# Performance work log

Hardware: AMD Instinct MI355X
Metric: run time of the kernel (lower is better)

The kernel has to match this reference:

```python
import jax, jax.numpy as jnp
import numpy as np

B, DM, DC, H = 16384, 1024, 8, 256  # batch, MRI feat dim, clinical feat dim, hidden_dim


def setup_inputs() -> dict:
    key = jax.random.key(0)
    ks = jax.random.split(key, 16)
    f = lambda k, s: jax.random.normal(k, s, dtype=jnp.float32)
    return {
        # encoder outputs (4 MRI modalities @1024-d, clinical @8-d)
        'feat_t1': f(ks[0], (B, DM)), 'feat_t1c': f(ks[1], (B, DM)),
        'feat_t2': f(ks[2], (B, DM)), 'feat_flair': f(ks[3], (B, DM)),
        'feat_cl': f(ks[4], (B, DC)),
        # per-modality projection Linears (MRI ones stacked: same math as 4 separate Linears)
        'Wp_mri': f(ks[5], (4, H, DM)) * 0.02, 'bp_mri': jnp.zeros((4, H), jnp.float32),
        'Wp_cl': f(ks[6], (H, DC)) * 0.02, 'bp_cl': jnp.zeros((H,), jnp.float32),
        # attention MLP: Linear(256,64) -> Tanh -> Linear(64,1)
        'Wa1': f(ks[7], (64, H)) * 0.02, 'ba1': jnp.zeros((64,), jnp.float32),
        'Wa2': f(ks[8], (1, 64)) * 0.02, 'ba2': jnp.zeros((1,), jnp.float32),
        # classifier: 256->128 LN ReLU -> 128->64 LN ReLU -> 64->1 (num_class-1)
        'Wc1': f(ks[9], (128, H)) * 0.02, 'bc1': jnp.zeros((128,), jnp.float32),
        'g1': jnp.ones((128,), jnp.float32), 'be1': jnp.zeros((128,), jnp.float32),
        'Wc2': f(ks[10], (64, 128)) * 0.02, 'bc2': jnp.zeros((64,), jnp.float32),
        'g2': jnp.ones((64,), jnp.float32), 'be2': jnp.zeros((64,), jnp.float32),
        'Wc3': f(ks[11], (1, 64)) * 0.02, 'bc3': jnp.zeros((1,), jnp.float32),
    }


def _ln(x, g, b, eps=1e-5):
    m = jnp.mean(x, axis=-1, keepdims=True)
    v = jnp.var(x, axis=-1, keepdims=True)
    return (x - m) * jax.lax.rsqrt(v + eps) * g + b


def reference(feat_t1, feat_t1c, feat_t2, feat_flair, feat_cl,
              Wp_mri, bp_mri, Wp_cl, bp_cl,
              Wa1, ba1, Wa2, ba2,
              Wc1, bc1, g1, be1, Wc2, bc2, g2, be2, Wc3, bc3):
    mri = jnp.stack([feat_t1, feat_t1c, feat_t2, feat_flair], axis=1)  # [B,4,DM]
    pm = jnp.einsum('bmd,mhd->bmh', mri, Wp_mri) + bp_mri              # [B,4,H] per-modality Linear
    pc = feat_cl @ Wp_cl.T + bp_cl                                     # [B,H]
    proj = jnp.concatenate([pm, pc[:, None, :]], axis=1)               # [B,5,H] == torch.stack(proj_feats, dim=1)
    scores = jnp.tanh(proj @ Wa1.T + ba1) @ Wa2.T + ba2                # [B,5,1]
    attn_weights = jax.nn.softmax(scores, axis=1)                      # softmax over modalities
    fused = jnp.sum(attn_weights * proj, axis=1)                       # [B,H]
    h = jax.nn.relu(_ln(fused @ Wc1.T + bc1, g1, be1))                 # dropout is identity in eval
    h = jax.nn.relu(_ln(h @ Wc2.T + bc2, g2, be2))
    out = h @ Wc3.T + bc3                                              # [B,1]
    return out, attn_weights
```

## Files before the change

### kernel.cpp

```cpp
#include <hip/hip_runtime.h>
#include <math.h>

typedef unsigned short u16;
typedef unsigned int   u32;
typedef __bf16 bf16x8 __attribute__((ext_vector_type(8)));
typedef float  f32x4  __attribute__((ext_vector_type(4)));
typedef u16    u16x8  __attribute__((ext_vector_type(8)));
typedef u16    u16x4  __attribute__((ext_vector_type(4)));

#define B_TOT 16384
#define DM_   1024
#define H_    256

#define WS_SCORES 41943040
#define WS_WP     42270720
#define WS_WA1    44367872
#define WS_WC1    44400640
#define WS_WC2    44466176

__device__ __forceinline__ u16 f2bf(float f){
  __bf16 h = (__bf16)f;
  return __builtin_bit_cast(u16, h);
}
__device__ __forceinline__ float bf2f(u16 h){
  return __builtin_bit_cast(float, ((u32)h) << 16);
}
__device__ __forceinline__ u16x4 cvt4(f32x4 a){
  u16x4 h;
  #pragma unroll
  for (int j = 0; j < 4; j++) h[j] = f2bf(a[j]);
  return h;
}
__device__ __forceinline__ f32x4 mfma16(bf16x8 a, bf16x8 b, f32x4 c){
  return __builtin_amdgcn_mfma_f32_16x16x32_bf16(a, b, c, 0, 0, 0);
}
__device__ __forceinline__ void glds16(const void* g, void* l){
  __builtin_amdgcn_global_load_lds(
      (const __attribute__((address_space(1))) void*)g,
      (__attribute__((address_space(3))) void*)l, 16, 0, 0);
}

__global__ void k0_convert(const float* __restrict__ s0, u16* __restrict__ d0, int n0,
                           const float* __restrict__ s1, u16* __restrict__ d1, int n1,
                           const float* __restrict__ s2, u16* __restrict__ d2, int n2,
                           const float* __restrict__ s3, u16* __restrict__ d3, int n3)
{
  int total4 = (n0 + n1 + n2 + n3) >> 2;
  for (int i = blockIdx.x * blockDim.x + threadIdx.x; i < total4; i += gridDim.x * blockDim.x){
    int e = i << 2;
    const float* s; u16* d; int off;
    if (e < n0)            { s = s0; d = d0; off = e; }
    else if (e < n0+n1)    { s = s1; d = d1; off = e - n0; }
    else if (e < n0+n1+n2) { s = s2; d = d2; off = e - n0 - n1; }
    else                   { s = s3; d = d3; off = e - n0 - n1 - n2; }
    f32x4 f = *(const f32x4*)(s + off);
    *(u16x4*)(d + off) = cvt4(f);
  }
}

__global__ __launch_bounds__(256) void k1b_clin(
    const float* __restrict__ fcl, const float* __restrict__ Wpcl, const float* __restrict__ bpcl,
    const u16* __restrict__ Wa1bf, const float* __restrict__ ba1,
    const float* __restrict__ Wa2, const float* __restrict__ ba2,
    u16* __restrict__ proj, float* __restrict__ scores)
{
  __shared__ u16 pcs[4][16*264];
  const int tid = threadIdx.x, lane = tid & 63, wv = tid >> 6;
  const int l15 = lane & 15, l4 = lane >> 4;
  const int rbase = blockIdx.x * 64 + wv * 16;

  f32x4 wA[4], wB[4];
  f32x4 bp = *(const f32x4*)(bpcl + lane * 4);
  #pragma unroll
  for (int c = 0; c < 4; c++){
    wA[c] = *(const f32x4*)(Wpcl + (lane*4 + c) * 8);
    wB[c] = *(const f32x4*)(Wpcl + (lane*4 + c) * 8 + 4);
  }
  #pragma unroll 4
  for (int r = 0; r < 16; r++){
    int row = rbase + r;
    f32x4 fA = *(const f32x4*)(fcl + (size_t)row * 8);
    f32x4 fB = *(const f32x4*)(fcl + (size_t)row * 8 + 4);
    u16x4 h;
    #pragma unroll
    for (int c = 0; c < 4; c++){
      float v = bp[c] + fA[0]*wA[c][0] + fA[1]*wA[c][1] + fA[2]*wA[c][2] + fA[3]*wA[c][3]
                      + fB[0]*wB[c][0] + fB[1]*wB[c][1] + fB[2]*wB[c][2] + fB[3]*wB[c][3];
      h[c] = f2bf(v);
    }
    *(u16x4*)(proj + (size_t)row * 1280 + 1024 + lane * 4) = h;
    *(u16x4*)(&pcs[wv][r * 264 + lane * 4]) = h;
  }
  f32x4 at[4];
  #pragma unroll
  for (int nf = 0; nf < 4; nf++) at[nf] = f32x4{0.f,0.f,0.f,0.f};
  #pragma unroll
  for (int kk = 0; kk < 8; kk++){
    bf16x8 a = *(const bf16x8*)((const char*)&pcs[wv][0] + l15*528 + kk*64 + l4*16);
    #pragma unroll
    for (int nf = 0; nf < 4; nf++){
      bf16x8 b = *(const bf16x8*)((const char*)Wa1bf + (nf*16 + l15)*512 + kk*64 + l4*16);
      at[nf] = mfma16(a, b, at[nf]);
    }
  }
  float po[4] = {0.f,0.f,0.f,0.f};
  #pragma unroll
  for (int nf = 0; nf < 4; nf++){
    int col = nf*16 + l15;
    float bb = ba1[col], w2 = Wa2[col];
    #pragma unroll
    for (int rg = 0; rg < 4; rg++) po[rg] += tanhf(at[nf][rg] + bb) * w2;
  }
  #pragma unroll
  for (int rg = 0; rg < 4; rg++){
    #pragma unroll
    for (int d = 1; d < 16; d <<= 1) po[rg] += __shfl_xor(po[rg], d);
  }
  if (l15 == 0){
    float b2 = ba2[0];
    #pragma unroll
    for (int rg = 0; rg < 4; rg++)
      scores[(size_t)(rbase + l4*4 + rg) * 5 + 4] = po[rg] + b2;
  }
}

__global__ __launch_bounds__(512, 4) void k1_proj(
    const float* __restrict__ ft1, const float* __restrict__ ft1c,
    const float* __restrict__ ft2, const float* __restrict__ ftfl,
    const u16* __restrict__ Wpbf, const float* __restrict__ bpm,
    const u16* __restrict__ Wa1bf, const float* __restrict__ ba1,
    const float* __restrict__ Wa2, const float* __restrict__ ba2,
    u16* __restrict__ proj, float* __restrict__ scores)
{
  extern __shared__ char lds[];
  const int bid = blockIdx.x;
  const int mm = (bid & 7) >> 1;
  const int bx = ((bid >> 3) << 1) | (bid & 1);
  const int b0 = bx * 64;
  const int tid = threadIdx.x;
  const int lane = tid & 63;
  const int wv = tid >> 6;
  const int l15 = lane & 15, l4 = lane >> 4;

  const float* Am = (mm == 0) ? ft1 : ((mm == 1) ? ft1c : ((mm == 2) ? ft2 : ftfl));
  const u16*   Wm = Wpbf + (size_t)mm * (H_ * DM_);
  const char*  Ab8 = (const char*)Am;

  const int a_r0 = tid >> 4;
  const int a_r1 = 32 + a_r0;
  const size_t a_src0 = (size_t)(b0 + a_r0) * 4096 + (size_t)((((tid & 15) * 16)) ^ ((a_r0 & 7) << 4));
  const size_t a_src1 = (size_t)(b0 + a_r1) * 4096 + (size_t)((((tid & 15) * 16)) ^ ((a_r1 & 7) << 4));
  const int a_dstw = wv * 1024;

  const u16* pW = Wm + (size_t)(wv*32 + l15) * DM_ + l4*8;

  u16x8 rW[2][4];
  f32x4 acc[4][2];
  #pragma unroll
  for (int i = 0; i < 4; i++)
    #pragma unroll
    for (int j = 0; j < 2; j++) acc[i][j] = f32x4{0.f,0.f,0.f,0.f};

  #pragma unroll
  for (int q = 0; q < 4; q++){
    int nf = q >> 1, kk = q & 1;
    rW[0][q] = *(const u16x8*)(pW + (size_t)nf*16*DM_ + kk*32);
  }
  #pragma unroll
  for (int t = 0; t < 3; t++){
    char* base = lds + t * 16384;
    glds16(Ab8 + a_src0 + (size_t)t * 256, base + a_dstw);
    glds16(Ab8 + a_src1 + (size_t)t * 256, base + 8192 + a_dstw);
  }

  #pragma unroll
  for (int c = 0; c < 16; ++c){
    asm volatile("s_waitcnt vmcnt(2)" ::: "memory");
    __builtin_amdgcn_sched_barrier(0);
    __builtin_amdgcn_s_barrier();
    __builtin_amdgcn_sched_barrier(0);
    if (c + 1 < 16){
      #pragma unroll
      for (int q = 0; q < 4; q++){
        int nf = q >> 1, kk = q & 1;
        rW[(c+1)&1][q] = *(const u16x8*)(pW + (size_t)nf*16*DM_ + (c+1)*64 + kk*32);
      }
    }
    if (c + 3 < 16){
      char* base = lds + ((c+3) & 3) * 16384;
      glds16(Ab8 + a_src0 + (size_t)(c+3) * 256, base + a_dstw);
      glds16(Ab8 + a_src1 + (size_t)(c+3) * 256, base + 8192 + a_dstw);
    }
    {
      const char* Abuf = lds + (c & 3) * 16384;
      #pragma unroll
      for (int kk = 0; kk < 2; kk++){
        bf16x8 af[4];
        #pragma unroll
        for (int mf = 0; mf < 4; mf++){
          int row = mf*16 + l15;
          int rb = row * 256;
          int sw = (row & 7) << 4;
          f32x4 x0 = *(const f32x4*)(Abuf + rb + ((kk*128 + l4*32) ^ sw));
          f32x4 x1 = *(const f32x4*)(Abuf + rb + ((kk*128 + l4*32 + 16) ^ sw));
          bf16x8 h;
          #pragma unroll
          for (int j = 0; j < 4; j++){ h[j] = (__bf16)x0[j]; h[4+j] = (__bf16)x1[j]; }
          af[mf] = h;
        }
        #pragma unroll
        for (int nf = 0; nf < 2; nf++){
          bf16x8 wf = __builtin_bit_cast(bf16x8, rW[c&1][nf*2 + kk]);
          #pragma unroll
          for (int mf = 0; mf < 4; mf++)
            acc[mf][nf] = mfma16(af[mf], wf, acc[mf][nf]);
        }
      }
    }
  }

  __syncthreads();

  {
    float bias[2];
    #pragma unroll
    for (int nf = 0; nf < 2; nf++) bias[nf] = bpm[mm*256 + wv*32 + nf*16 + l15];
    #pragma unroll
    for (int mf = 0; mf < 4; mf++){
      #pragma unroll
      for (int nf = 0; nf < 2; nf++){
        int cc = wv*32 + nf*16 + l15;
        #pragma unroll
        for (int rg = 0; rg < 4; rg++){
          int r = mf*16 + l4*4 + rg;
          *(u16*)(lds + r*512 + ((cc*2) ^ ((r & 7) << 4))) = f2bf(acc[mf][nf][rg] + bias[nf]);
        }
      }
    }
  }
  __syncthreads();

  #pragma unroll
  for (int i = 0; i < 4; i++){
    int q = i*512 + tid;
    int r = q >> 5, cc = q & 31;
    u16x8 v = *(const u16x8*)(lds + r*512 + ((cc*16) ^ ((r & 7) << 4)));
    *(u16x8*)((char*)proj + (size_t)(b0 + r) * 2560 + mm*512 + cc*16) = v;
  }
  if (wv < 4){
    f32x4 a2[4];
    #pragma unroll
    for (int nf = 0; nf < 4; nf++) a2[nf] = f32x4{0.f,0.f,0.f,0.f};
    #pragma unroll
    for (int kk = 0; kk < 8; kk++){
      int kb = kk*64 + l4*16;
      int r = wv*16 + l15;
      bf16x8 afr = *(const bf16x8*)(lds + r*512 + (kb ^ ((r & 7) << 4)));
      #pragma unroll
      for (int nf = 0; nf < 4; nf++){
        int n = nf*16 + l15;
        bf16x8 bfr = *(const bf16x8*)((const char*)Wa1bf + n*512 + kb);
        a2[nf] = mfma16(afr, bfr, a2[nf]);
      }
    }
    float p0 = 0.f, p1 = 0.f, p2 = 0.f, p3 = 0.f;
    #pragma unroll
    for (int nf = 0; nf < 4; nf++){
      int n = nf*16 + l15;
      float w2 = Wa2[n], bn = ba1[n];
      p0 += tanhf(a2[nf][0] + bn) * w2;
      p1 += tanhf(a2[nf][1] + bn) * w2;
      p2 += tanhf(a2[nf][2] + bn) * w2;
      p3 += tanhf(a2[nf][3] + bn) * w2;
    }
    #pragma unroll
    for (int d = 1; d < 16; d <<= 1){
      p0 += __shfl_xor(p0, d); p1 += __shfl_xor(p1, d);
      p2 += __shfl_xor(p2, d); p3 += __shfl_xor(p3, d);
    }
    if (l15 == 0){
      float bav = ba2[0];
      int rb = wv*16 + l4*4;
      scores[(size_t)(b0 + rb + 0)*5 + mm] = p0 + bav;
      scores[(size_t)(b0 + rb + 1)*5 + mm] = p1 + bav;
      scores[(size_t)(b0 + rb + 2)*5 + mm] = p2 + bav;
      scores[(size_t)(b0 + rb + 3)*5 + mm] = p3 + bav;
    }
  }
}

__global__ __launch_bounds__(256) void k2_cls(
    const u16* __restrict__ proj, const float* __restrict__ scores,
    const u16* __restrict__ Wc1bf, const u16* __restrict__ Wc2bf,
    const float* __restrict__ bc1, const float* __restrict__ g1, const float* __restrict__ be1,
    const float* __restrict__ bc2, const float* __restrict__ g2, const float* __restrict__ be2,
    const float* __restrict__ Wc3, const float* __restrict__ bc3,
    float* __restrict__ outp)
{
  __shared__ u16 h1s[4][16*136];
  const int tid = threadIdx.x, lane = tid & 63, wv = tid >> 6;
  const int l15 = lane & 15, l4 = lane >> 4;
  const int b0 = blockIdx.x * 64;
  const int rowA = b0 + wv*16 + l15;

  const float* sc = scores + (size_t)rowA * 5;
  float s0 = sc[0], s1 = sc[1], s2 = sc[2], s3 = sc[3], s4 = sc[4];
  float mx = fmaxf(fmaxf(fmaxf(s0, s1), fmaxf(s2, s3)), s4);
  float e0 = expf(s0-mx), e1 = expf(s1-mx), e2 = expf(s2-mx), e3 = expf(s3-mx), e4 = expf(s4-mx);
  float inv = 1.0f / (e0 + e1 + e2 + e3 + e4);
  float w0 = e0*inv, w1 = e1*inv, w2 = e2*inv, w3 = e3*inv, w4 = e4*inv;
  if (l4 == 0){
    float* ap = outp + B_TOT + (size_t)rowA * 5;
    ap[0] = w0; ap[1] = w1; ap[2] = w2; ap[3] = w3; ap[4] = w4;
  }

  bf16x8 af[8];
  const u16* pr = proj + (size_t)rowA * 1280 + l4*8;
  #pragma unroll
  for (int kk = 0; kk < 8; kk++){
    u16x8 p0v = *(const u16x8*)(pr + kk*32);
    u16x8 p1v = *(const u16x8*)(pr + 256  + kk*32);
    u16x8 p2v = *(const u16x8*)(pr + 512  + kk*32);
    u16x8 p3v = *(const u16x8*)(pr + 768  + kk*32);
    u16x8 p4v = *(const u16x8*)(pr + 1024 + kk*32);
    bf16x8 a;
    #pragma unroll
    for (int j = 0; j < 8; j++)
      a[j] = (__bf16)(w0*bf2f(p0v[j]) + w1*bf2f(p1v[j]) + w2*bf2f(p2v[j])
                    + w3*bf2f(p3v[j]) + w4*bf2f(p4v[j]));
    af[kk] = a;
  }

  f32x4 acc1[8];
  #pragma unroll
  for (int of = 0; of < 8; of++) acc1[of] = f32x4{0.f,0.f,0.f,0.f};
  #pragma unroll
  for (int kk = 0; kk < 8; kk++){
    #pragma unroll
    for (int of = 0; of < 8; of++){
      bf16x8 b = *(const bf16x8*)((const char*)Wc1bf + (of*16 + l15)*512 + kk*64 + l4*16);
      acc1[of] = mfma16(af[kk], b, acc1[of]);
    }
  }
  float sum1[4] = {0.f,0.f,0.f,0.f};
  #pragma unroll
  for (int of = 0; of < 8; of++){
    float bb = bc1[of*16 + l15];
    #pragma unroll
    for (int rg = 0; rg < 4; rg++){ acc1[of][rg] += bb; sum1[rg] += acc1[of][rg]; }
  }
  #pragma unroll
  for (int rg = 0; rg < 4; rg++){
    #pragma unroll
    for (int d = 1; d < 16; d <<= 1) sum1[rg] += __shfl_xor(sum1[rg], d);
  }
  float vs1[4] = {0.f,0.f,0.f,0.f};
  float mean1[4];
  #pragma unroll
  for (int rg = 0; rg < 4; rg++) mean1[rg] = sum1[rg] * 0.0078125f;
  #pragma unroll
  for (int of = 0; of < 8; of++)
    #pragma unroll
    for (int rg = 0; rg < 4; rg++){ float dd = acc1[of][rg] - mean1[rg]; vs1[rg] += dd*dd; }
  #pragma unroll
  for (int rg = 0; rg < 4; rg++){
    #pragma unroll
    for (int d = 1; d < 16; d <<= 1) vs1[rg] += __shfl_xor(vs1[rg], d);
  }
  float is1[4];
  #pragma unroll
  for (int rg = 0; rg < 4; rg++) is1[rg] = rsqrtf(vs1[rg] * 0.0078125f + 1e-5f);
  #pragma unroll
  for (int of = 0; of < 8; of++){
    int col = of*16 + l15;
    float gg = g1[col], bb = be1[col];
    #pragma unroll
    for (int rg = 0; rg < 4; rg++){
      float h = fmaxf((acc1[of][rg] - mean1[rg]) * is1[rg] * gg + bb, 0.f);
      h1s[wv][(l4*4 + rg)*136 + col] = f2bf(h);
    }
  }

  f32x4 acc2[4];
  #pragma unroll
  for (int of = 0; of < 4; of++) acc2[of] = f32x4{0.f,0.f,0.f,0.f};
  #pragma unroll
  for (int kk = 0; kk < 4; kk++){
    bf16x8 a2 = *(const bf16x8*)((const char*)&h1s[wv][0] + l15*272 + kk*64 + l4*16);
    #pragma unroll
    for (int of = 0; of < 4; of++){
      bf16x8 b = *(const bf16x8*)((const char*)Wc2bf + (of*16 + l15)*256 + kk*64 + l4*16);
      acc2[of] = mfma16(a2, b, acc2[of]);
    }
  }
  float sum2[4] = {0.f,0.f,0.f,0.f};
  #pragma unroll
  for (int of = 0; of < 4; of++){
    float bb = bc2[of*16 + l15];
    #pragma unroll
    for (int rg = 0; rg < 4; rg++){ acc2[of][rg] += bb; sum2[rg] += acc2[of][rg]; }
  }
  #pragma unroll
  for (int rg = 0; rg < 4; rg++){
    #pragma unroll
    for (int d = 1; d < 16; d <<= 1) sum2[rg] += __shfl_xor(sum2[rg], d);
  }
  float mean2[4], vs2[4] = {0.f,0.f,0.f,0.f};
  #pragma unroll
  for (int rg = 0; rg < 4; rg++) mean2[rg] = sum2[rg] * 0.015625f;
  #pragma unroll
  for (int of = 0; of < 4; of++)
    #pragma unroll
    for (int rg = 0; rg < 4; rg++){ float dd = acc2[of][rg] - mean2[rg]; vs2[rg] += dd*dd; }
  #pragma unroll
  for (int rg = 0; rg < 4; rg++){
    #pragma unroll
    for (int d = 1; d < 16; d <<= 1) vs2[rg] += __shfl_xor(vs2[rg], d);
  }
  float po[4] = {0.f,0.f,0.f,0.f};
  #pragma unroll
  for (int of = 0; of < 4; of++){
    int col = of*16 + l15;
    float gg = g2[col], bb = be2[col], w3c = Wc3[col];
    #pragma unroll
    for (int rg = 0; rg < 4; rg++){
      float is2 = rsqrtf(vs2[rg] * 0.015625f + 1e-5f);
      float h = fmaxf((acc2[of][rg] - mean2[rg]) * is2 * gg + bb, 0.f);
      po[rg] += h * w3c;
    }
  }
  #pragma unroll
  for (int rg = 0; rg < 4; rg++){
    #pragma unroll
    for (int d = 1; d < 16; d <<= 1) po[rg] += __shfl_xor(po[rg], d);
  }
  if (l15 == 0){
    float b3 = bc3[0];
    #pragma unroll
    for (int rg = 0; rg < 4; rg++)
      outp[b0 + wv*16 + l4*4 + rg] = po[rg] + b3;
  }
}

extern "C" void kernel_launch(void* const* d_in, const int* in_sizes, int n_in,
                              void* d_out, int out_size, void* d_ws, size_t ws_size,
                              hipStream_t stream)
{
  (void)in_sizes; (void)n_in; (void)out_size; (void)ws_size;
  const float* ft1  = (const float*)d_in[0];
  const float* ft1c = (const float*)d_in[1];
  const float* ft2  = (const float*)d_in[2];
  const float* ftfl = (const float*)d_in[3];
  const float* fcl  = (const float*)d_in[4];
  const float* Wpmri= (const float*)d_in[5];
  const float* bpm  = (const float*)d_in[6];
  const float* Wpcl = (const float*)d_in[7];
  const float* bpcl = (const float*)d_in[8];
  const float* Wa1  = (const float*)d_in[9];
  const float* ba1  = (const float*)d_in[10];
  const float* Wa2  = (const float*)d_in[11];
  const float* ba2  = (const float*)d_in[12];
  const float* Wc1  = (const float*)d_in[13];
  const float* bc1  = (const float*)d_in[14];
  const float* g1   = (const float*)d_in[15];
  const float* be1  = (const float*)d_in[16];
  const float* Wc2  = (const float*)d_in[17];
  const float* bc2  = (const float*)d_in[18];
  const float* g2   = (const float*)d_in[19];
  const float* be2  = (const float*)d_in[20];
  const float* Wc3  = (const float*)d_in[21];
  const float* bc3  = (const float*)d_in[22];
  float* outp = (float*)d_out;
  char* ws = (char*)d_ws;

  u16*   proj   = (u16*)(ws);
  float* scores = (float*)(ws + WS_SCORES);
  u16*   Wpbf   = (u16*)(ws + WS_WP);
  u16*   Wa1bf  = (u16*)(ws + WS_WA1);
  u16*   Wc1bf  = (u16*)(ws + WS_WC1);
  u16*   Wc2bf  = (u16*)(ws + WS_WC2);

  (void)hipFuncSetAttribute((const void*)k1_proj, hipFuncAttributeMaxDynamicSharedMemorySize, 65536);

  k0_convert<<<dim3(512), dim3(256), 0, stream>>>(
      Wpmri, Wpbf, 4 * H_ * DM_,
      Wa1,  Wa1bf, 64 * H_,
      Wc1,  Wc1bf, 128 * H_,
      Wc2,  Wc2bf, 64 * 128);

  k1b_clin<<<dim3(256), dim3(256), 0, stream>>>(
      fcl, Wpcl, bpcl, Wa1bf, ba1, Wa2, ba2, proj, scores);

  k1_proj<<<dim3(1024), dim3(512), 65536, stream>>>(
      ft1, ft1c, ft2, ftfl, Wpbf, bpm, Wa1bf, ba1, Wa2, ba2, proj, scores);

  k2_cls<<<dim3(256), dim3(256), 0, stream>>>(
      proj, scores, Wc1bf, Wc2bf, bc1, g1, be1, bc2, g2, be2, Wc3, bc3, outp);
}
```

Measured before the change: 146.4 us.

## Restructure projection GEMM pipeline into four big double-buffered K chunks

The projection kernel's K loop changes from 16 small 256-byte chunks with a 4-deep LDS ring to 4 large 1024-byte chunks, double-buffered in 128KB of LDS. Weight fragments for a whole chunk are held in registers and loaded after each chunk's compute. The aim is fewer barriers and larger transfers per stage. In exchange it doubles LDS per block and lowers launch-bound occupancy from 4 to 2, which may cut the latency hiding that came from running more blocks at once.

```diff
diff --git a/kernel.cpp b/kernel.cpp
--- a/kernel.cpp
+++ b/kernel.cpp
@@ -124,7 +124,7 @@
   }
 }
 
-__global__ __launch_bounds__(512, 4) void k1_proj(
+__global__ __launch_bounds__(512, 2) void k1_proj(
     const float* __restrict__ ft1, const float* __restrict__ ft1c,
     const float* __restrict__ ft2, const float* __restrict__ ftfl,
     const u16* __restrict__ Wpbf, const float* __restrict__ bpm,
@@ -146,63 +146,56 @@
   const u16*   Wm = Wpbf + (size_t)mm * (H_ * DM_);
   const char*  Ab8 = (const char*)Am;
 
-  const int a_r0 = tid >> 4;
-  const int a_r1 = 32 + a_r0;
-  const size_t a_src0 = (size_t)(b0 + a_r0) * 4096 + (size_t)((((tid & 15) * 16)) ^ ((a_r0 & 7) << 4));
-  const size_t a_src1 = (size_t)(b0 + a_r1) * 4096 + (size_t)((((tid & 15) * 16)) ^ ((a_r1 & 7) << 4));
-  const int a_dstw = wv * 1024;
-
   const u16* pW = Wm + (size_t)(wv*32 + l15) * DM_ + l4*8;
 
-  u16x8 rW[2][4];
+  u16x8 rW[8][2];
   f32x4 acc[4][2];
   #pragma unroll
   for (int i = 0; i < 4; i++)
     #pragma unroll
     for (int j = 0; j < 2; j++) acc[i][j] = f32x4{0.f,0.f,0.f,0.f};
 
-  #pragma unroll
-  for (int q = 0; q < 4; q++){
-    int nf = q >> 1, kk = q & 1;
-    rW[0][q] = *(const u16x8*)(pW + (size_t)nf*16*DM_ + kk*32);
-  }
-  #pragma unroll
-  for (int t = 0; t < 3; t++){
-    char* base = lds + t * 16384;
-    glds16(Ab8 + a_src0 + (size_t)t * 256, base + a_dstw);
-    glds16(Ab8 + a_src1 + (size_t)t * 256, base + 8192 + a_dstw);
-  }
-
-  #pragma unroll
-  for (int c = 0; c < 16; ++c){
-    asm volatile("s_waitcnt vmcnt(2)" ::: "memory");
+  #define K1_LOADW(c) do{                                                   \
+    _Pragma("unroll")                                                       \
+    for (int ks = 0; ks < 8; ks++){                                         \
+      rW[ks][0] = *(const u16x8*)(pW + (c)*256 + ks*32);                    \
+      rW[ks][1] = *(const u16x8*)(pW + (size_t)16*DM_ + (c)*256 + ks*32);   \
+    }                                                                       \
+  } while(0)
+  #define K1_STAGE(c) do{                                                   \
+    char* buf_ = lds + ((c) & 1) * 65536;                                   \
+    _Pragma("unroll")                                                       \
+    for (int j = 0; j < 8; j++){                                            \
+      int r_ = j*8 + wv;                                                    \
+      glds16(Ab8 + (size_t)(b0 + r_)*4096 + (size_t)(c)*1024               \
+                 + (size_t)((lane*16) ^ ((r_ & 7) << 4)),                   \
+             buf_ + r_*1024);                                               \
+    }                                                                       \
+  } while(0)
+
+  K1_LOADW(0);
+  K1_STAGE(0);
+
+  #pragma unroll
+  for (int c = 0; c < 4; ++c){
+    if (c < 3) K1_STAGE(c + 1);
+    __builtin_amdgcn_sched_barrier(0);
+    if (c < 3) asm volatile("s_waitcnt vmcnt(8)" ::: "memory");
+    else       asm volatile("s_waitcnt vmcnt(0)" ::: "memory");
     __builtin_amdgcn_sched_barrier(0);
     __builtin_amdgcn_s_barrier();
     __builtin_amdgcn_sched_barrier(0);
-    if (c + 1 < 16){
+    {
+      const char* buf = lds + (c & 1) * 65536;
       #pragma unroll
-      for (int q = 0; q < 4; q++){
-        int nf = q >> 1, kk = q & 1;
-        rW[(c+1)&1][q] = *(const u16x8*)(pW + (size_t)nf*16*DM_ + (c+1)*64 + kk*32);
-      }
-    }
-    if (c + 3 < 16){
-      char* base = lds + ((c+3) & 3) * 16384;
-      glds16(Ab8 + a_src0 + (size_t)(c+3) * 256, base + a_dstw);
-      glds16(Ab8 + a_src1 + (size_t)(c+3) * 256, base + 8192 + a_dstw);
-    }
-    {
-      const char* Abuf = lds + (c & 3) * 16384;
-      #pragma unroll
-      for (int kk = 0; kk < 2; kk++){
+      for (int ks = 0; ks < 8; ks++){
         bf16x8 af[4];
         #pragma unroll
         for (int mf = 0; mf < 4; mf++){
           int row = mf*16 + l15;
-          int rb = row * 256;
           int sw = (row & 7) << 4;
-          f32x4 x0 = *(const f32x4*)(Abuf + rb + ((kk*128 + l4*32) ^ sw));
-          f32x4 x1 = *(const f32x4*)(Abuf + rb + ((kk*128 + l4*32 + 16) ^ sw));
+          f32x4 x0 = *(const f32x4*)(buf + row*1024 + ((ks*128 + l4*32) ^ sw));
+          f32x4 x1 = *(const f32x4*)(buf + row*1024 + ((ks*128 + l4*32 + 16) ^ sw));
           bf16x8 h;
           #pragma unroll
           for (int j = 0; j < 4; j++){ h[j] = (__bf16)x0[j]; h[4+j] = (__bf16)x1[j]; }
@@ -210,16 +203,20 @@
         }
         #pragma unroll
         for (int nf = 0; nf < 2; nf++){
-          bf16x8 wf = __builtin_bit_cast(bf16x8, rW[c&1][nf*2 + kk]);
+          bf16x8 wf = __builtin_bit_cast(bf16x8, rW[ks][nf]);
           #pragma unroll
           for (int mf = 0; mf < 4; mf++)
             acc[mf][nf] = mfma16(af[mf], wf, acc[mf][nf]);
         }
       }
     }
-  }
-
-  __syncthreads();
+    if (c < 3) K1_LOADW(c + 1);
+    __builtin_amdgcn_sched_barrier(0);
+    __builtin_amdgcn_s_barrier();
+    __builtin_amdgcn_sched_barrier(0);
+  }
+  #undef K1_LOADW
+  #undef K1_STAGE
 
   {
     float bias[2];
@@ -480,7 +477,7 @@
   u16*   Wc1bf  = (u16*)(ws + WS_WC1);
   u16*   Wc2bf  = (u16*)(ws + WS_WC2);
 
-  (void)hipFuncSetAttribute((const void*)k1_proj, hipFuncAttributeMaxDynamicSharedMemorySize, 65536);
+  (void)hipFuncSetAttribute((const void*)k1_proj, hipFuncAttributeMaxDynamicSharedMemorySize, 131072);
 
   k0_convert<<<dim3(512), dim3(256), 0, stream>>>(
       Wpmri, Wpbf, 4 * H_ * DM_,
@@ -491,7 +488,7 @@
   k1b_clin<<<dim3(256), dim3(256), 0, stream>>>(
       fcl, Wpcl, bpcl, Wa1bf, ba1, Wa2, ba2, proj, scores);
 
-  k1_proj<<<dim3(1024), dim3(512), 65536, stream>>>(
+  k1_proj<<<dim3(1024), dim3(512), 131072, stream>>>(
       ft1, ft1c, ft2, ftfl, Wpbf, bpm, Wa1bf, ba1, Wa2, ba2, proj, scores);
 
   k2_cls<<<dim3(256), dim3(256), 0, stream>>>(
```

New measurement: 177.7 us. 21.4% more time.

## Pre-convert MRI features to swizzled bf16 and stage both GEMM operands via LDS

Applied to the files above, without the earlier changes.

Adds a pre-pass kernel that converts the four fp32 MRI feature matrices into a swizzled bf16 workspace layout, and stores the projection weights in the same swizzled layout. The projection GEMM then loads both A and W tiles into LDS with async global-to-LDS copies in a 3-stage pipeline, using larger 128x256 tiles and removing in-loop fp32-to-bf16 conversion. This trades extra HBM traffic (writing and rereading a bf16 copy of the activations) for a simpler, denser MFMA inner loop. A per-modality fallback runs when the workspace is too small.

```diff
diff --git a/kernel.cpp b/kernel.cpp
--- a/kernel.cpp
+++ b/kernel.cpp
@@ -17,7 +17,13 @@
 #define WS_WA1    44367872
 #define WS_WC1    44400640
 #define WS_WC2    44466176
-
+#define WS_ABF    50331648
+#define NEED_BATCH  184549376ull
+#define NEED_SINGLE  83886080ull
+
+__device__ __forceinline__ size_t swz(int row, int boff){
+  return (size_t)row * 2048 + (size_t)(boff ^ ((row & 7) << 4));
+}
 __device__ __forceinline__ u16 f2bf(float f){
   __bf16 h = (__bf16)f;
   return __builtin_bit_cast(u16, h);
@@ -38,6 +44,21 @@
   __builtin_amdgcn_global_load_lds(
       (const __attribute__((address_space(1))) void*)g,
       (__attribute__((address_space(3))) void*)l, 16, 0, 0);
+}
+
+__global__ __launch_bounds__(256) void k_cvt(
+    const float* __restrict__ s0, const float* __restrict__ s1,
+    const float* __restrict__ s2, const float* __restrict__ s3,
+    u16* __restrict__ dst, int n4)
+{
+  const int stride = gridDim.x * blockDim.x;
+  for (int i = blockIdx.x * blockDim.x + threadIdx.x; i < n4; i += stride){
+    int m = i >> 22, local = i & 4194303;
+    const float* s = (m == 0) ? s0 : ((m == 1) ? s1 : ((m == 2) ? s2 : s3));
+    f32x4 v = *(const f32x4*)(s + (size_t)local * 4);
+    int row = local >> 8, boff = (local & 255) * 8;
+    *(u16x4*)((char*)dst + (size_t)m * 33554432 + swz(row, boff)) = cvt4(v);
+  }
 }
 
 __global__ void k0_convert(const float* __restrict__ s0, u16* __restrict__ d0, int n0,
@@ -48,13 +69,18 @@
   int total4 = (n0 + n1 + n2 + n3) >> 2;
   for (int i = blockIdx.x * blockDim.x + threadIdx.x; i < total4; i += gridDim.x * blockDim.x){
     int e = i << 2;
-    const float* s; u16* d; int off;
-    if (e < n0)            { s = s0; d = d0; off = e; }
-    else if (e < n0+n1)    { s = s1; d = d1; off = e - n0; }
-    else if (e < n0+n1+n2) { s = s2; d = d2; off = e - n0 - n1; }
-    else                   { s = s3; d = d3; off = e - n0 - n1 - n2; }
-    f32x4 f = *(const f32x4*)(s + off);
-    *(u16x4*)(d + off) = cvt4(f);
+    if (e < n0){
+      f32x4 f = *(const f32x4*)(s0 + e);
+      int row = e >> 10, boff = (e & 1023) * 2;
+      *(u16x4*)((char*)d0 + swz(row, boff)) = cvt4(f);
+    } else {
+      const float* s; u16* d; int off;
+      if (e < n0+n1)         { s = s1; d = d1; off = e - n0; }
+      else if (e < n0+n1+n2) { s = s2; d = d2; off = e - n0 - n1; }
+      else                   { s = s3; d = d3; off = e - n0 - n1 - n2; }
+      f32x4 f = *(const f32x4*)(s + off);
+      *(u16x4*)(d + off) = cvt4(f);
+    }
   }
 }
 
@@ -125,114 +151,94 @@
 }
 
 __global__ __launch_bounds__(512, 4) void k1_proj(
-    const float* __restrict__ ft1, const float* __restrict__ ft1c,
-    const float* __restrict__ ft2, const float* __restrict__ ftfl,
-    const u16* __restrict__ Wpbf, const float* __restrict__ bpm,
+    const u16* __restrict__ Abf, const u16* __restrict__ Wpbf,
+    const float* __restrict__ bpm,
     const u16* __restrict__ Wa1bf, const float* __restrict__ ba1,
     const float* __restrict__ Wa2, const float* __restrict__ ba2,
-    u16* __restrict__ proj, float* __restrict__ scores)
+    u16* __restrict__ proj, float* __restrict__ scores, int mmFixed)
 {
   extern __shared__ char lds[];
   const int bid = blockIdx.x;
-  const int mm = (bid & 7) >> 1;
-  const int bx = ((bid >> 3) << 1) | (bid & 1);
-  const int b0 = bx * 64;
+  int mm, bx;
+  if (mmFixed < 0){ mm = (bid & 7) >> 1; bx = ((bid >> 3) << 1) | (bid & 1); }
+  else            { mm = mmFixed;        bx = bid; }
+  const int b0 = bx * 128;
   const int tid = threadIdx.x;
   const int lane = tid & 63;
   const int wv = tid >> 6;
+  const int wm = wv >> 2, wn = wv & 3;
   const int l15 = lane & 15, l4 = lane >> 4;
 
-  const float* Am = (mm == 0) ? ft1 : ((mm == 1) ? ft1c : ((mm == 2) ? ft2 : ftfl));
-  const u16*   Wm = Wpbf + (size_t)mm * (H_ * DM_);
-  const char*  Ab8 = (const char*)Am;
-
-  const int a_r0 = tid >> 4;
-  const int a_r1 = 32 + a_r0;
-  const size_t a_src0 = (size_t)(b0 + a_r0) * 4096 + (size_t)((((tid & 15) * 16)) ^ ((a_r0 & 7) << 4));
-  const size_t a_src1 = (size_t)(b0 + a_r1) * 4096 + (size_t)((((tid & 15) * 16)) ^ ((a_r1 & 7) << 4));
+  const char* Ap = (const char*)Abf + (mmFixed < 0 ? (size_t)mm * 33554432 : 0);
+  const char* Wp = (const char*)Wpbf;
+
+  const int a_c16 = tid >> 7, a_r = tid & 127;
   const int a_dstw = wv * 1024;
-
-  const u16* pW = Wm + (size_t)(wv*32 + l15) * DM_ + l4*8;
-
-  u16x8 rW[2][4];
-  f32x4 acc[4][2];
+  int w_c16[2], w_col[2];
+  #pragma unroll
+  for (int i = 0; i < 2; i++){ int q = i*512 + tid; w_c16[i] = q >> 8; w_col[i] = q & 255; }
+
+  f32x4 acc[4][4];
   #pragma unroll
   for (int i = 0; i < 4; i++)
     #pragma unroll
-    for (int j = 0; j < 2; j++) acc[i][j] = f32x4{0.f,0.f,0.f,0.f};
-
-  #pragma unroll
-  for (int q = 0; q < 4; q++){
-    int nf = q >> 1, kk = q & 1;
-    rW[0][q] = *(const u16x8*)(pW + (size_t)nf*16*DM_ + kk*32);
-  }
-  #pragma unroll
-  for (int t = 0; t < 3; t++){
-    char* base = lds + t * 16384;
-    glds16(Ab8 + a_src0 + (size_t)t * 256, base + a_dstw);
-    glds16(Ab8 + a_src1 + (size_t)t * 256, base + 8192 + a_dstw);
-  }
-
-  #pragma unroll
-  for (int c = 0; c < 16; ++c){
-    asm volatile("s_waitcnt vmcnt(2)" ::: "memory");
+    for (int j = 0; j < 4; j++) acc[i][j] = f32x4{0.f,0.f,0.f,0.f};
+
+  auto stage = [&](int kt, int sb){
+    glds16(Ap + swz(b0 + a_r, kt*64 + a_c16*16), lds + sb + a_dstw);
+    #pragma unroll
+    for (int i = 0; i < 2; i++){
+      int gr = mm*256 + w_col[i];
+      glds16(Wp + swz(gr, kt*64 + w_c16[i]*16), lds + sb + 8192 + i*8192 + a_dstw);
+    }
+  };
+  auto compute = [&](int sb){
+    const char* Ab = lds + sb;
+    const char* Wb = lds + sb + 8192;
+    bf16x8 af[4];
+    #pragma unroll
+    for (int mf = 0; mf < 4; mf++)
+      af[mf] = *(const bf16x8*)(Ab + l4*2048 + (wm*64 + mf*16 + l15)*16);
+    #pragma unroll
+    for (int nf = 0; nf < 4; nf++){
+      bf16x8 wf = *(const bf16x8*)(Wb + l4*4096 + (wn*64 + nf*16 + l15)*16);
+      #pragma unroll
+      for (int mf = 0; mf < 4; mf++)
+        acc[mf][nf] = mfma16(af[mf], wf, acc[mf][nf]);
+    }
+  };
+
+  stage(0, 0);
+  stage(1, 24576);
+  int curB = 0, stgB = 49152;
+  for (int kt = 0; kt < 31; ++kt){
+    asm volatile("s_waitcnt vmcnt(3)" ::: "memory");
     __builtin_amdgcn_sched_barrier(0);
     __builtin_amdgcn_s_barrier();
     __builtin_amdgcn_sched_barrier(0);
-    if (c + 1 < 16){
-      #pragma unroll
-      for (int q = 0; q < 4; q++){
-        int nf = q >> 1, kk = q & 1;
-        rW[(c+1)&1][q] = *(const u16x8*)(pW + (size_t)nf*16*DM_ + (c+1)*64 + kk*32);
-      }
-    }
-    if (c + 3 < 16){
-      char* base = lds + ((c+3) & 3) * 16384;
-      glds16(Ab8 + a_src0 + (size_t)(c+3) * 256, base + a_dstw);
-      glds16(Ab8 + a_src1 + (size_t)(c+3) * 256, base + 8192 + a_dstw);
-    }
-    {
-      const char* Abuf = lds + (c & 3) * 16384;
-      #pragma unroll
-      for (int kk = 0; kk < 2; kk++){
-        bf16x8 af[4];
-        #pragma unroll
-        for (int mf = 0; mf < 4; mf++){
-          int row = mf*16 + l15;
-          int rb = row * 256;
-          int sw = (row & 7) << 4;
-          f32x4 x0 = *(const f32x4*)(Abuf + rb + ((kk*128 + l4*32) ^ sw));
-          f32x4 x1 = *(const f32x4*)(Abuf + rb + ((kk*128 + l4*32 + 16) ^ sw));
-          bf16x8 h;
-          #pragma unroll
-          for (int j = 0; j < 4; j++){ h[j] = (__bf16)x0[j]; h[4+j] = (__bf16)x1[j]; }
-          af[mf] = h;
-        }
-        #pragma unroll
-        for (int nf = 0; nf < 2; nf++){
-          bf16x8 wf = __builtin_bit_cast(bf16x8, rW[c&1][nf*2 + kk]);
-          #pragma unroll
-          for (int mf = 0; mf < 4; mf++)
-            acc[mf][nf] = mfma16(af[mf], wf, acc[mf][nf]);
-        }
-      }
-    }
-  }
-
+    if (kt + 2 < 32) stage(kt + 2, stgB);
+    compute(curB);
+    int nb = curB + 24576; curB = (nb == 73728) ? 0 : nb;
+    int ns = stgB + 24576; stgB = (ns == 73728) ? 0 : ns;
+  }
+  asm volatile("s_waitcnt vmcnt(0)" ::: "memory");
+  __builtin_amdgcn_s_barrier();
+  __builtin_amdgcn_sched_barrier(0);
+  compute(curB);
   __syncthreads();
 
   {
-    float bias[2];
-    #pragma unroll
-    for (int nf = 0; nf < 2; nf++) bias[nf] = bpm[mm*256 + wv*32 + nf*16 + l15];
+    float bias[4];
+    #pragma unroll
+    for (int nf = 0; nf < 4; nf++) bias[nf] = bpm[mm*256 + wn*64 + nf*16 + l15];
     #pragma unroll
     for (int mf = 0; mf < 4; mf++){
       #pragma unroll
-      for (int nf = 0; nf < 2; nf++){
-        int cc = wv*32 + nf*16 + l15;
+      for (int nf = 0; nf < 4; nf++){
+        int cc = wn*64 + nf*16 + l15;
         #pragma unroll
         for (int rg = 0; rg < 4; rg++){
-          int r = mf*16 + l4*4 + rg;
+          int r = wm*64 + mf*16 + l4*4 + rg;
           *(u16*)(lds + r*512 + ((cc*2) ^ ((r & 7) << 4))) = f2bf(acc[mf][nf][rg] + bias[nf]);
         }
       }
@@ -241,13 +247,13 @@
   __syncthreads();
 
   #pragma unroll
-  for (int i = 0; i < 4; i++){
+  for (int i = 0; i < 8; i++){
     int q = i*512 + tid;
     int r = q >> 5, cc = q & 31;
     u16x8 v = *(const u16x8*)(lds + r*512 + ((cc*16) ^ ((r & 7) << 4)));
     *(u16x8*)((char*)proj + (size_t)(b0 + r) * 2560 + mm*512 + cc*16) = v;
   }
-  if (wv < 4){
+  {
     f32x4 a2[4];
     #pragma unroll
     for (int nf = 0; nf < 4; nf++) a2[nf] = f32x4{0.f,0.f,0.f,0.f};
@@ -446,7 +452,7 @@
                               void* d_out, int out_size, void* d_ws, size_t ws_size,
                               hipStream_t stream)
 {
-  (void)in_sizes; (void)n_in; (void)out_size; (void)ws_size;
+  (void)in_sizes; (void)n_in; (void)out_size;
   const float* ft1  = (const float*)d_in[0];
   const float* ft1c = (const float*)d_in[1];
   const float* ft2  = (const float*)d_in[2];
@@ -479,8 +485,9 @@
   u16*   Wa1bf  = (u16*)(ws + WS_WA1);
   u16*   Wc1bf  = (u16*)(ws + WS_WC1);
   u16*   Wc2bf  = (u16*)(ws + WS_WC2);
-
-  (void)hipFuncSetAttribute((const void*)k1_proj, hipFuncAttributeMaxDynamicSharedMemorySize, 65536);
+  u16*   Abf    = (u16*)(ws + WS_ABF);
+
+  (void)hipFuncSetAttribute((const void*)k1_proj, hipFuncAttributeMaxDynamicSharedMemorySize, 73728);
 
   k0_convert<<<dim3(512), dim3(256), 0, stream>>>(
       Wpmri, Wpbf, 4 * H_ * DM_,
@@ -491,8 +498,19 @@
   k1b_clin<<<dim3(256), dim3(256), 0, stream>>>(
       fcl, Wpcl, bpcl, Wa1bf, ba1, Wa2, ba2, proj, scores);
 
-  k1_proj<<<dim3(1024), dim3(512), 65536, stream>>>(
-      ft1, ft1c, ft2, ftfl, Wpbf, bpm, Wa1bf, ba1, Wa2, ba2, proj, scores);
+  if (ws_size >= NEED_BATCH){
+    k_cvt<<<dim3(2048), dim3(256), 0, stream>>>(ft1, ft1c, ft2, ftfl, Abf, 16777216);
+    k1_proj<<<dim3(512), dim3(512), 73728, stream>>>(
+        Abf, Wpbf, bpm, Wa1bf, ba1, Wa2, ba2, proj, scores, -1);
+  } else {
+    const float* srcs[4] = {ft1, ft1c, ft2, ftfl};
+    for (int m = 0; m < 4; m++){
+      k_cvt<<<dim3(2048), dim3(256), 0, stream>>>(
+          srcs[m], srcs[m], srcs[m], srcs[m], Abf, 4194304);
+      k1_proj<<<dim3(128), dim3(512), 73728, stream>>>(
+          Abf, Wpbf, bpm, Wa1bf, ba1, Wa2, ba2, proj, scores, m);
+    }
+  }
 
   k2_cls<<<dim3(256), dim3(256), 0, stream>>>(
       proj, scores, Wc1bf, Wc2bf, bc1, g1, be1, bc2, g2, be2, Wc3, bc3, outp);
```

After: 194.6 us. 1.33x slower.
